# Kernel optimization log

Hardware: AMD Instinct MI355X
Metric: run time of the kernel (lower is better)

The kernel has to match this reference:

```python
import jax, jax.numpy as jnp
import numpy as np

B, W, N = 128, 128, 64
HID = 150  # lstm_hid_dim == recon_hid_dim
L = 2      # layer_numb


def _edges_fc(n):
    # for j in range(n) for i in range(n) if i != j -> row0 = i (src), row1 = j (dst)
    a = np.arange(n)
    src = np.concatenate([np.delete(a, j) for j in range(n)])
    dst = np.repeat(a, n - 1)
    return np.stack([src, dst]).astype(np.int32)


def _edges_tc(w):
    # for j in range(w) for i in range(j) -> row0 = i (src), row1 = j (dst)
    src = np.concatenate([np.arange(j) for j in range(1, w)])
    dst = np.repeat(np.arange(w), np.arange(w))
    return np.stack([src, dst]).astype(np.int32)


def _batch_edges(e, b, n):
    # tile per-graph edges b times with node offsets (block-diagonal batched graph)
    off = (jnp.arange(b) * n).astype(e.dtype)
    return (e[:, None, :] + off[None, :, None]).reshape(2, -1)


def _gat_conv(x, edge_index, w, a_src, a_dst, b):
    # PyG GATConv, heads=1: h = x W^T; e_ij = LeakyReLU(a_src.h_j + a_dst.h_i); softmax over dst
    m = x.shape[0]
    loop = jnp.arange(m, dtype=edge_index.dtype)
    src = jnp.concatenate([edge_index[0], loop])
    dst = jnp.concatenate([edge_index[1], loop])
    h = x @ w.T
    e = jax.nn.leaky_relu(h @ a_src, 0.2)[src] + jax.nn.leaky_relu(jnp.zeros((), h.dtype), 0.2) * 0
    e = jax.nn.leaky_relu((h @ a_src)[src] + (h @ a_dst)[dst], 0.2)
    emax = jax.ops.segment_max(e, dst, num_segments=m)
    ex = jnp.exp(e - emax[dst])
    denom = jax.ops.segment_sum(ex, dst, num_segments=m)
    alpha = ex / denom[dst]
    out = jax.ops.segment_sum(h[src] * alpha[:, None], dst, num_segments=m)
    return out + b


def _gcn_conv(x, edge_index, w, b):
    # PyG GCNConv: add self loops, D^{-1/2} A D^{-1/2} (x W^T) + b
    m = x.shape[0]
    loop = jnp.arange(m, dtype=edge_index.dtype)
    src = jnp.concatenate([edge_index[0], loop])
    dst = jnp.concatenate([edge_index[1], loop])
    h = x @ w.T
    deg = jax.ops.segment_sum(jnp.ones(src.shape, h.dtype), dst, num_segments=m)
    dinv = 1.0 / jnp.sqrt(deg)
    norm = dinv[src] * dinv[dst]
    out = jax.ops.segment_sum(h[src] * norm[:, None], dst, num_segments=m)
    return out + b


def _stgat_block(x, fc_e, tc_e, gw, gas, gad, gb, cw, cb):
    x = jax.lax.stop_gradient(x)  # data.clone().detach()
    b, w, n = x.shape
    xp = jnp.transpose(x, (0, 2, 1)).reshape(-1, w)          # [B*N, W]
    f = jax.nn.relu(_gat_conv(xp, fc_e, gw, gas, gad, gb))
    f = f.reshape(b, n, w)
    z = jnp.transpose(f, (0, 2, 1)).reshape(-1, n)           # [B*W, N]
    t = jax.nn.relu(_gcn_conv(z, tc_e, cw, cb))
    t = t.reshape(b, n, w)  # faithful to torch view(B, node_num, -1) quirk
    return jnp.transpose(t, (0, 2, 1))


def _conv_branch(x, w, b, k):
    pad = (k - 1) // 2
    xc = jnp.transpose(x, (0, 2, 1))  # [B, N, W]
    xc = jnp.pad(xc, ((0, 0), (0, 0), (pad, pad)))
    y = jax.lax.conv_general_dilated(xc, w, (1,), 'VALID',
                                     dimension_numbers=('NCH', 'OIH', 'NCH'))
    y = jax.nn.relu(y + b[None, :, None])
    return jnp.transpose(y, (0, 2, 1))


def _lstm_scan(x, w_ih, w_hh, b_ih, b_hh, reverse):
    hdim = w_hh.shape[1]

    def step(carry, xt):
        h, c = carry
        g = xt @ w_ih.T + h @ w_hh.T + b_ih + b_hh
        i, f, gg, o = jnp.split(g, 4, axis=-1)
        c = jax.nn.sigmoid(f) * c + jax.nn.sigmoid(i) * jnp.tanh(gg)
        h = jax.nn.sigmoid(o) * jnp.tanh(c)
        return (h, c), h

    bsz = x.shape[0]
    init = (jnp.zeros((bsz, hdim), x.dtype), jnp.zeros((bsz, hdim), x.dtype))
    xs = jnp.swapaxes(x, 0, 1)  # [T, B, D]
    _, hs = jax.lax.scan(step, init, xs, reverse=reverse)
    return jnp.swapaxes(hs, 0, 1)  # [B, T, H]


def reference(x, fc_edge_index, tc_edge_index,
              conv2_w, conv2_b, conv3_w, conv3_b,
              gat_w, gat_asrc, gat_adst, gat_b, gcn_w, gcn_b,
              lstm_wih, lstm_whh, lstm_bih, lstm_bhh,
              dec_wih, dec_whh, dec_bih, dec_bhh, fc_w, fc_b):
    b, w, n = x.shape
    fc_e = _batch_edges(fc_edge_index, b, n)
    tc_e = _batch_edges(tc_edge_index, b, w)
    hs = [x, _conv_branch(x, conv2_w, conv2_b, 5), _conv_branch(x, conv3_w, conv3_b, 7)]
    nlayers = gat_w.shape[1]
    for t in range(3):
        for l in range(nlayers):
            hs[t] = hs[t] + _stgat_block(hs[t], fc_e, tc_e,
                                         gat_w[t, l], gat_asrc[t, l], gat_adst[t, l],
                                         gat_b[t, l], gcn_w[t, l], gcn_b[t, l])
    h = jnp.concatenate(hs, axis=2)  # [B, W, 3N]
    fwd = _lstm_scan(h, lstm_wih[0], lstm_whh[0], lstm_bih[0], lstm_bhh[0], False)
    bwd = _lstm_scan(h, lstm_wih[1], lstm_whh[1], lstm_bih[1], lstm_bhh[1], True)
    h_end = jnp.concatenate([fwd[:, -1], bwd[:, -1]], axis=-1)  # [B, 2H]
    rep = jnp.repeat(h_end, w, axis=1).reshape(b, w, -1)  # repeat_interleave + view quirk
    dfwd = _lstm_scan(rep, dec_wih[0], dec_whh[0], dec_bih[0], dec_bhh[0], False)
    dbwd = _lstm_scan(rep, dec_wih[1], dec_whh[1], dec_bih[1], dec_bhh[1], True)
    dec = jnp.concatenate([dfwd, dbwd], axis=-1)  # [B, W, 2H]
    return dec @ fc_w.T + fc_b


def setup_inputs() -> dict:
    key = jax.random.key(0)
    ks = jax.random.split(key, 24)
    s = 0.05
    f = lambda k, shp: jax.random.normal(k, shp, jnp.float32) * s
    return {
        'x': jax.random.normal(ks[0], (B, W, N), jnp.float32),
        'fc_edge_index': jnp.asarray(_edges_fc(N)),
        'tc_edge_index': jnp.asarray(_edges_tc(W)),
        'conv2_w': f(ks[1], (N, N, 5)), 'conv2_b': f(ks[2], (N,)),
        'conv3_w': f(ks[3], (N, N, 7)), 'conv3_b': f(ks[4], (N,)),
        'gat_w': f(ks[5], (3, L, W, W)), 'gat_asrc': f(ks[6], (3, L, W)),
        'gat_adst': f(ks[7], (3, L, W)), 'gat_b': f(ks[8], (3, L, W)),
        'gcn_w': f(ks[9], (3, L, N, N)), 'gcn_b': f(ks[10], (3, L, N)),
        'lstm_wih': f(ks[11], (2, 4 * HID, 3 * N)), 'lstm_whh': f(ks[12], (2, 4 * HID, HID)),
        'lstm_bih': f(ks[13], (2, 4 * HID)), 'lstm_bhh': f(ks[14], (2, 4 * HID)),
        'dec_wih': f(ks[15], (2, 4 * HID, 2 * HID)), 'dec_whh': f(ks[16], (2, 4 * HID, HID)),
        'dec_bih': f(ks[17], (2, 4 * HID)), 'dec_bhh': f(ks[18], (2, 4 * HID)),
        'fc_w': f(ks[19], (N, 2 * HID)), 'fc_b': f(ks[20], (N,)),
    }
```

## Files before the change

kernel.cpp:

```cpp
#include <hip/hip_runtime.h>
#include <hip/hip_fp16.h>


typedef _Float16 v2h __attribute__((ext_vector_type(2)));

__device__ __forceinline__ float sigm(float x) {
    return 1.0f / (1.0f + __expf(-x));
}
__device__ __forceinline__ float tanhfast(float x) {
    return 2.0f / (1.0f + __expf(-2.0f * x)) - 1.0f;
}
__device__ __forceinline__ v2h pk2(float a, float b) {
    v2h r; r[0] = (_Float16)a; r[1] = (_Float16)b; return r;
}
__device__ __forceinline__ unsigned pku(float a, float b) {
    return __builtin_bit_cast(unsigned, pk2(a, b));
}
__device__ __forceinline__ v2h upk(unsigned u) { return __builtin_bit_cast(v2h, u); }
__device__ __forceinline__ float fdot2(v2h a, v2h b, float c) {
#if __has_builtin(__builtin_amdgcn_fdot2)
    return __builtin_amdgcn_fdot2(a, b, c, false);
#else
    return c + (float)a[0] * (float)b[0] + (float)a[1] * (float)b[1];
#endif
}

__device__ __forceinline__ void barrier_lds() {
    asm volatile("s_waitcnt lgkmcnt(0)" ::: "memory");
    __builtin_amdgcn_s_barrier();
}

__global__ void k_copy(const float* __restrict__ x, float* __restrict__ hs0) {
    int i = blockIdx.x * 256 + threadIdx.x;
    ((float4*)hs0)[i] = ((const float4*)x)[i];
}

__global__ __launch_bounds__(256) void k_conv2(
    const float* __restrict__ x,
    const float* __restrict__ cw5, const float* __restrict__ cb5,
    const float* __restrict__ cw7, const float* __restrict__ cb7,
    float* __restrict__ hs1, float* __restrict__ hs2) {
    extern __shared__ float S[];
    float* xt = S;
    float* wl = S + 70 * 68;
    int b = blockIdx.x, wh = blockIdx.y, br = blockIdx.z;
    int K = br ? 7 : 5;
    const float* cw = br ? cw7 : cw5;
    const float* cb = br ? cb7 : cb5;
    float* dst = br ? hs2 : hs1;
    int w0 = wh * 64;
    int tid = threadIdx.x;

    for (int f = tid; f < 70 * 64; f += 256) {
        int ww = f >> 6, i = f & 63;
        int wp = w0 - 3 + ww;
        xt[ww * 68 + i] = ((unsigned)wp < 128u) ? x[b * 8192 + wp * 64 + i] : 0.f;
    }
    int nw = K * 4096;
    for (int f = tid; f < nw; f += 256) {
        int j = f & 3, o = (f >> 2) & 63, i4 = (f >> 8) & 15, t = f >> 12;
        wl[f] = cw[(o * 64 + i4 * 4 + j) * K + t];
    }
    __syncthreads();

    int to = tid & 15, tw = tid >> 4;
    float acc[4][4] = {};
    int ob = 3 - (K >> 1);
    for (int t = 0; t < K; ++t) {
        int rbase = tw * 4 + t + ob;
        for (int i4 = 0; i4 < 16; ++i4) {
            float4 a0 = *(const float4*)&xt[(rbase + 0) * 68 + i4 * 4];
            float4 a1 = *(const float4*)&xt[(rbase + 1) * 68 + i4 * 4];
            float4 a2 = *(const float4*)&xt[(rbase + 2) * 68 + i4 * 4];
            float4 a3 = *(const float4*)&xt[(rbase + 3) * 68 + i4 * 4];
            const float* wrow = &wl[(t * 16 + i4) * 256];
            float4 b0 = *(const float4*)&wrow[to * 4];
            float4 b1 = *(const float4*)&wrow[(to + 16) * 4];
            float4 b2 = *(const float4*)&wrow[(to + 32) * 4];
            float4 b3 = *(const float4*)&wrow[(to + 48) * 4];
            #define DOT4(w_, a_) \
                acc[w_][0] = fmaf(a_.x, b0.x, acc[w_][0]); acc[w_][0] = fmaf(a_.y, b0.y, acc[w_][0]); \
                acc[w_][0] = fmaf(a_.z, b0.z, acc[w_][0]); acc[w_][0] = fmaf(a_.w, b0.w, acc[w_][0]); \
                acc[w_][1] = fmaf(a_.x, b1.x, acc[w_][1]); acc[w_][1] = fmaf(a_.y, b1.y, acc[w_][1]); \
                acc[w_][1] = fmaf(a_.z, b1.z, acc[w_][1]); acc[w_][1] = fmaf(a_.w, b1.w, acc[w_][1]); \
                acc[w_][2] = fmaf(a_.x, b2.x, acc[w_][2]); acc[w_][2] = fmaf(a_.y, b2.y, acc[w_][2]); \
                acc[w_][2] = fmaf(a_.z, b2.z, acc[w_][2]); acc[w_][2] = fmaf(a_.w, b2.w, acc[w_][2]); \
                acc[w_][3] = fmaf(a_.x, b3.x, acc[w_][3]); acc[w_][3] = fmaf(a_.y, b3.y, acc[w_][3]); \
                acc[w_][3] = fmaf(a_.z, b3.z, acc[w_][3]); acc[w_][3] = fmaf(a_.w, b3.w, acc[w_][3]);
            DOT4(0, a0)
            DOT4(1, a1)
            DOT4(2, a2)
            DOT4(3, a3)
            #undef DOT4
        }
    }
    #pragma unroll
    for (int wj = 0; wj < 4; ++wj) {
        int w = w0 + tw * 4 + wj;
        #pragma unroll
        for (int oj = 0; oj < 4; ++oj) {
            int o = to + 16 * oj;
            dst[b * 8192 + w * 64 + o] = fmaxf(acc[wj][oj] + cb[o], 0.f);
        }
    }
}

__global__ __launch_bounds__(256, 2) void k_stgat(
    float* __restrict__ hs0, float* __restrict__ hs1, float* __restrict__ hs2,
    const float* __restrict__ gat_w, const float* __restrict__ gat_asrc,
    const float* __restrict__ gat_adst, const float* __restrict__ gat_b,
    const float* __restrict__ gcn_w, const float* __restrict__ gcn_b, int l) {
    extern __shared__ float S[];
    _Float16* Sh = (_Float16*)S;
    const int XHh = 0;
    const int GHh = 8448;
    const int HHTh = 25344;
    const int AHh = 34560;
    const int FHh = 8448;
    const int CHh = 0;
    const int SDo = 17024;
    const int CSo = 17024;
    const int HGo = 8576;

    int b = blockIdx.x, br = blockIdx.y, tid = threadIdx.x;
    float* hs = (br == 0 ? hs0 : (br == 1 ? hs1 : hs2)) + b * 8192;
    int wsel = br * 2 + l;
    const float* gw = gat_w + wsel * 16384;
    const float* asr = gat_asrc + wsel * 128;
    const float* ads = gat_adst + wsel * 128;
    const float* gb = gat_b + wsel * 128;
    const float* cwp = gcn_w + wsel * 4096;
    const float* cbp = gcn_b + wsel * 64;

    {
        const float4* hsv = (const float4*)hs;
        for (int mt = tid; mt < 512; mt += 256) {
            int ng = mt & 15, wg = mt >> 4;
            float4 r0 = hsv[(wg * 4 + 0) * 16 + ng];
            float4 r1 = hsv[(wg * 4 + 1) * 16 + ng];
            float4 r2 = hsv[(wg * 4 + 2) * 16 + ng];
            float4 r3 = hsv[(wg * 4 + 3) * 16 + ng];
            int n0 = ng * 4, ww = wg * 4;
            *(uint2*)&Sh[XHh + (n0 + 0) * 132 + ww] = make_uint2(pku(r0.x, r1.x), pku(r2.x, r3.x));
            *(uint2*)&Sh[XHh + (n0 + 1) * 132 + ww] = make_uint2(pku(r0.y, r1.y), pku(r2.y, r3.y));
            *(uint2*)&Sh[XHh + (n0 + 2) * 132 + ww] = make_uint2(pku(r0.z, r1.z), pku(r2.z, r3.z));
            *(uint2*)&Sh[XHh + (n0 + 3) * 132 + ww] = make_uint2(pku(r0.w, r1.w), pku(r2.w, r3.w));
        }
        const float4* gwv = (const float4*)gw;
        for (int f4 = tid; f4 < 4096; f4 += 256) {
            float4 v = gwv[f4];
            int wo = f4 >> 5, k4 = f4 & 31;
            *(uint2*)&Sh[GHh + wo * 132 + k4 * 4] = make_uint2(pku(v.x, v.y), pku(v.z, v.w));
        }
    }
    __syncthreads();

    int wq = tid & 15, nq = tid >> 4;
    {
        float asv[8], adv[8];
        #pragma unroll
        for (int c = 0; c < 8; ++c) { asv[c] = asr[wq + 16 * c]; adv[c] = ads[wq + 16 * c]; }
        float acc0[8] = {}, acc1[8] = {}, acc2[8] = {}, acc3[8] = {};
        const _Float16* Arow = Sh + XHh + nq * 4 * 132;
        const _Float16* Brow = Sh + GHh + wq * 132;
        for (int k4 = 0; k4 < 32; ++k4) {
            uint2 u0 = *(const uint2*)&Arow[k4 * 4];
            uint2 u1 = *(const uint2*)&Arow[132 + k4 * 4];
            uint2 u2 = *(const uint2*)&Arow[264 + k4 * 4];
            uint2 u3 = *(const uint2*)&Arow[396 + k4 * 4];
            v2h a0l = upk(u0.x), a0h = upk(u0.y), a1l = upk(u1.x), a1h = upk(u1.y);
            v2h a2l = upk(u2.x), a2h = upk(u2.y), a3l = upk(u3.x), a3h = upk(u3.y);
            #pragma unroll
            for (int c = 0; c < 8; ++c) {
                uint2 ub = *(const uint2*)&Brow[c * (16 * 132) + k4 * 4];
                v2h bl = upk(ub.x), bh = upk(ub.y);
                acc0[c] = fdot2(a0l, bl, acc0[c]); acc0[c] = fdot2(a0h, bh, acc0[c]);
                acc1[c] = fdot2(a1l, bl, acc1[c]); acc1[c] = fdot2(a1h, bh, acc1[c]);
                acc2[c] = fdot2(a2l, bl, acc2[c]); acc2[c] = fdot2(a2h, bh, acc2[c]);
                acc3[c] = fdot2(a3l, bl, acc3[c]); acc3[c] = fdot2(a3h, bh, acc3[c]);
            }
        }
        #pragma unroll
        for (int c = 0; c < 8; ++c)
            *(uint2*)&Sh[HHTh + (wq + 16 * c) * 68 + nq * 4] =
                make_uint2(pku(acc0[c], acc1[c]), pku(acc2[c], acc3[c]));
        float ps0 = 0, ps1 = 0, ps2 = 0, ps3 = 0, pd0 = 0, pd1 = 0, pd2 = 0, pd3 = 0;
        #pragma unroll
        for (int c = 0; c < 8; ++c) {
            ps0 = fmaf(acc0[c], asv[c], ps0); ps1 = fmaf(acc1[c], asv[c], ps1);
            ps2 = fmaf(acc2[c], asv[c], ps2); ps3 = fmaf(acc3[c], asv[c], ps3);
            pd0 = fmaf(acc0[c], adv[c], pd0); pd1 = fmaf(acc1[c], adv[c], pd1);
            pd2 = fmaf(acc2[c], adv[c], pd2); pd3 = fmaf(acc3[c], adv[c], pd3);
        }
        #pragma unroll
        for (int m = 1; m < 16; m <<= 1) {
            ps0 += __shfl_xor(ps0, m); ps1 += __shfl_xor(ps1, m);
            ps2 += __shfl_xor(ps2, m); ps3 += __shfl_xor(ps3, m);
            pd0 += __shfl_xor(pd0, m); pd1 += __shfl_xor(pd1, m);
            pd2 += __shfl_xor(pd2, m); pd3 += __shfl_xor(pd3, m);
        }
        if (wq == 0) {
            S[SDo + nq * 4 + 0] = ps0; S[SDo + nq * 4 + 1] = ps1;
            S[SDo + nq * 4 + 2] = ps2; S[SDo + nq * 4 + 3] = ps3;
            S[SDo + 64 + nq * 4 + 0] = pd0; S[SDo + 64 + nq * 4 + 1] = pd1;
            S[SDo + 64 + nq * 4 + 2] = pd2; S[SDo + 64 + nq * 4 + 3] = pd3;
        }
    }
    __syncthreads();

    {
        const float4* cwv = (const float4*)cwp;
        for (int f4 = tid; f4 < 1024; f4 += 256) {
            float4 v = cwv[f4];
            int c = f4 >> 4, k4 = f4 & 15;
            *(uint2*)&Sh[CHh + c * 68 + k4 * 4] = make_uint2(pku(v.x, v.y), pku(v.z, v.w));
        }
        if (tid < 64) {
            int j = tid;
            float dj = S[SDo + 64 + j];
            float mx = -1e30f;
            for (int i = 0; i < 64; ++i) {
                float e = S[SDo + i] + dj;
                e = (e > 0.f) ? e : 0.2f * e;
                mx = fmaxf(mx, e);
            }
            float sum = 0.f;
            for (int i = 0; i < 64; i += 2) {
                float e0 = S[SDo + i] + dj;     e0 = (e0 > 0.f) ? e0 : 0.2f * e0;
                float e1 = S[SDo + i + 1] + dj; e1 = (e1 > 0.f) ? e1 : 0.2f * e1;
                float x0 = __expf(e0 - mx), x1 = __expf(e1 - mx);
                sum += x0 + x1;
                *(unsigned*)&Sh[AHh + j * 68 + i] = pku(x0, x1);
            }
            float rinv = 1.f / sum;
            for (int i = 0; i < 64; i += 2) {
                v2h v = upk(*(const unsigned*)&Sh[AHh + j * 68 + i]);
                *(unsigned*)&Sh[AHh + j * 68 + i] = pku((float)v[0] * rinv, (float)v[1] * rinv);
            }
        }
    }
    __syncthreads();

    {
        float gbv[8];
        #pragma unroll
        for (int c = 0; c < 8; ++c) gbv[c] = gb[wq + 16 * c];
        float acc0[8] = {}, acc1[8] = {}, acc2[8] = {}, acc3[8] = {};
        const _Float16* Arow = Sh + AHh + nq * 4 * 68;
        const _Float16* Brow = Sh + HHTh + wq * 68;
        for (int k4 = 0; k4 < 16; ++k4) {
            uint2 u0 = *(const uint2*)&Arow[k4 * 4];
            uint2 u1 = *(const uint2*)&Arow[68 + k4 * 4];
            uint2 u2 = *(const uint2*)&Arow[136 + k4 * 4];
            uint2 u3 = *(const uint2*)&Arow[204 + k4 * 4];
            v2h a0l = upk(u0.x), a0h = upk(u0.y), a1l = upk(u1.x), a1h = upk(u1.y);
            v2h a2l = upk(u2.x), a2h = upk(u2.y), a3l = upk(u3.x), a3h = upk(u3.y);
            #pragma unroll
            for (int c = 0; c < 8; ++c) {
                uint2 ub = *(const uint2*)&Brow[c * (16 * 68) + k4 * 4];
                v2h bl = upk(ub.x), bh = upk(ub.y);
                acc0[c] = fdot2(a0l, bl, acc0[c]); acc0[c] = fdot2(a0h, bh, acc0[c]);
                acc1[c] = fdot2(a1l, bl, acc1[c]); acc1[c] = fdot2(a1h, bh, acc1[c]);
                acc2[c] = fdot2(a2l, bl, acc2[c]); acc2[c] = fdot2(a2h, bh, acc2[c]);
                acc3[c] = fdot2(a3l, bl, acc3[c]); acc3[c] = fdot2(a3h, bh, acc3[c]);
            }
        }
        #pragma unroll
        for (int c = 0; c < 8; ++c) {
            float f0 = fmaxf(acc0[c] + gbv[c], 0.f);
            float f1 = fmaxf(acc1[c] + gbv[c], 0.f);
            float f2 = fmaxf(acc2[c] + gbv[c], 0.f);
            float f3 = fmaxf(acc3[c] + gbv[c], 0.f);
            *(uint2*)&Sh[FHh + (wq + 16 * c) * 68 + nq * 4] = make_uint2(pku(f0, f1), pku(f2, f3));
        }
    }
    __syncthreads();

    {
        int cq = tid & 7, wg = tid >> 3;
        float acc0[8] = {}, acc1[8] = {}, acc2[8] = {}, acc3[8] = {};
        const _Float16* Arow = Sh + FHh + wg * 4 * 68;
        const _Float16* Brow = Sh + CHh + cq * 68;
        for (int k4 = 0; k4 < 16; ++k4) {
            uint2 u0 = *(const uint2*)&Arow[k4 * 4];
            uint2 u1 = *(const uint2*)&Arow[68 + k4 * 4];
            uint2 u2 = *(const uint2*)&Arow[136 + k4 * 4];
            uint2 u3 = *(const uint2*)&Arow[204 + k4 * 4];
            v2h a0l = upk(u0.x), a0h = upk(u0.y), a1l = upk(u1.x), a1h = upk(u1.y);
            v2h a2l = upk(u2.x), a2h = upk(u2.y), a3l = upk(u3.x), a3h = upk(u3.y);
            #pragma unroll
            for (int cc = 0; cc < 8; ++cc) {
                uint2 ub = *(const uint2*)&Brow[cc * (8 * 68) + k4 * 4];
                v2h bl = upk(ub.x), bh = upk(ub.y);
                acc0[cc] = fdot2(a0l, bl, acc0[cc]); acc0[cc] = fdot2(a0h, bh, acc0[cc]);
                acc1[cc] = fdot2(a1l, bl, acc1[cc]); acc1[cc] = fdot2(a1h, bh, acc1[cc]);
                acc2[cc] = fdot2(a2l, bl, acc2[cc]); acc2[cc] = fdot2(a2h, bh, acc2[cc]);
                acc3[cc] = fdot2(a3l, bl, acc3[cc]); acc3[cc] = fdot2(a3h, bh, acc3[cc]);
            }
        }
        #pragma unroll
        for (int cc = 0; cc < 8; ++cc) {
            int c = cq + 8 * cc;
            S[HGo + (wg * 4 + 0) * 66 + c] = acc0[cc];
            S[HGo + (wg * 4 + 1) * 66 + c] = acc1[cc];
            S[HGo + (wg * 4 + 2) * 66 + c] = acc2[cc];
            S[HGo + (wg * 4 + 3) * 66 + c] = acc3[cc];
        }
    }
    __syncthreads();

    {
        int c = tid & 63, q = tid >> 6;
        float local = 0.f;
        for (int i = 0; i < 32; ++i) {
            int w = q * 32 + i;
            local = fmaf(rsqrtf((float)(w + 1)), S[HGo + w * 66 + c], local);
        }
        S[CSo + q * 64 + c] = local;
    }
    __syncthreads();
    {
        int c = tid & 63, q = tid >> 6;
        float run = 0.f;
        for (int qq = 0; qq < q; ++qq) run += S[CSo + qq * 64 + c];
        float cbv = cbp[c];
        for (int i = 0; i < 32; ++i) {
            int w = q * 32 + i;
            float dv = rsqrtf((float)(w + 1));
            run = fmaf(dv, S[HGo + w * 66 + c], run);
            S[HGo + w * 66 + c] = fmaxf(fmaf(dv, run, cbv), 0.f);
        }
    }
    __syncthreads();

    {
        float4* hsv4 = (float4*)hs;
        for (int f4 = tid; f4 < 2048; f4 += 256) {
            int a = f4 >> 4, cc0 = (f4 & 15) * 4;
            float4 old = hsv4[f4];
            int n = a & 63, ahi = a >> 6;
            old.x += S[HGo + (cc0 * 2 + ahi) * 66 + n];
            old.y += S[HGo + ((cc0 + 1) * 2 + ahi) * 66 + n];
            old.z += S[HGo + ((cc0 + 2) * 2 + ahi) * 66 + n];
            old.w += S[HGo + ((cc0 + 3) * 2 + ahi) * 66 + n];
            hsv4[f4] = old;
        }
    }
}

__global__ __launch_bounds__(256) void k_encgemm2(
    const float* __restrict__ hs0, const float* __restrict__ hs1, const float* __restrict__ hs2,
    const float* __restrict__ wih, const float* __restrict__ bih, const float* __restrict__ bhh,
    float* __restrict__ gx0) {
    __shared__ __align__(16) _Float16 Xh[128 * 72];
    __shared__ __align__(16) _Float16 Wh[128 * 72];
    int b = blockIdx.x, gy = blockIdx.y, tid = threadIdx.x;
    int g0 = gy * 128;
    int ty = tid >> 4, tx = tid & 15;
    float acc[8][8];
    #pragma unroll
    for (int i = 0; i < 8; ++i)
        #pragma unroll
        for (int j = 0; j < 8; ++j) acc[i][j] = 0.f;
    const float* hsb[3] = {hs0 + b * 8192, hs1 + b * 8192, hs2 + b * 8192};

    for (int c = 0; c < 3; ++c) {
        const float4* src = (const float4*)hsb[c];
        for (int f = tid; f < 2048; f += 256) {
            int t = f >> 4, k4 = f & 15;
            float4 v = src[f];
            int pos = (((k4 >> 1) ^ ((t >> 3) & 7)) << 1) + (k4 & 1);
            *(uint2*)&Xh[t * 72 + pos * 4] = make_uint2(pku(v.x, v.y), pku(v.z, v.w));
        }
        for (int f = tid; f < 2048; f += 256) {
            int g = f >> 4, k4 = f & 15;
            int gg = g0 + g;
            float4 v = (gg < 600) ? *(const float4*)&wih[gg * 192 + c * 64 + k4 * 4]
                                  : make_float4(0.f, 0.f, 0.f, 0.f);
            int pos = (((k4 >> 1) ^ ((g >> 3) & 7)) << 1) + (k4 & 1);
            *(uint2*)&Wh[g * 72 + pos * 4] = make_uint2(pku(v.x, v.y), pku(v.z, v.w));
        }
        __syncthreads();
        #pragma unroll
        for (int k8 = 0; k8 < 8; ++k8) {
            uint4 av[8];
            #pragma unroll
            for (int i = 0; i < 8; ++i) {
                int row = ty * 8 + i;
                av[i] = *(const uint4*)&Xh[row * 72 + (k8 ^ ((row >> 3) & 7)) * 8];
            }
            #pragma unroll
            for (int j = 0; j < 8; ++j) {
                int row = tx * 8 + j;
                uint4 bv = *(const uint4*)&Wh[row * 72 + (k8 ^ ((row >> 3) & 7)) * 8];
                v2h b0 = upk(bv.x), b1 = upk(bv.y), b2 = upk(bv.z), b3 = upk(bv.w);
                #pragma unroll
                for (int i = 0; i < 8; ++i) {
                    acc[i][j] = fdot2(upk(av[i].x), b0, acc[i][j]);
                    acc[i][j] = fdot2(upk(av[i].y), b1, acc[i][j]);
                    acc[i][j] = fdot2(upk(av[i].z), b2, acc[i][j]);
                    acc[i][j] = fdot2(upk(av[i].w), b3, acc[i][j]);
                }
            }
        }
        __syncthreads();
    }
    #pragma unroll
    for (int i = 0; i < 8; ++i) {
        int t = ty * 8 + i;
        float* orow = gx0 + (b * 128 + t) * 600;
        #pragma unroll
        for (int jj = 0; jj < 2; ++jj) {
            int gbase = g0 + tx * 8 + jj * 4;
            if (gbase + 3 < 600) {
                float4 o;
                o.x = acc[i][jj * 4 + 0] + bih[gbase + 0] + bhh[gbase + 0];
                o.y = acc[i][jj * 4 + 1] + bih[gbase + 1] + bhh[gbase + 1];
                o.z = acc[i][jj * 4 + 2] + bih[gbase + 2] + bhh[gbase + 2];
                o.w = acc[i][jj * 4 + 3] + bih[gbase + 3] + bhh[gbase + 3];
                *(float4*)&orow[gbase] = o;
            } else {
                for (int e = 0; e < 4; ++e) {
                    int g = gbase + e;
                    if (g < 600) orow[g] = acc[i][jj * 4 + e] + bih[g] + bhh[g];
                }
            }
        }
    }
}

__global__ void k_encgx1(const float* __restrict__ hs0, const float* __restrict__ hs1,
                         const float* __restrict__ hs2, const float* __restrict__ wih,
                         const float* __restrict__ bih, const float* __restrict__ bhh,
                         float* __restrict__ gx1) {
    __shared__ __align__(16) float sh[192];
    int b = blockIdx.x, tid = threadIdx.x;
    if (tid < 192) {
        const float* src = (tid < 64 ? hs0 : (tid < 128 ? hs1 : hs2));
        sh[tid] = src[b * 8192 + 127 * 64 + (tid & 63)];
    }
    __syncthreads();
    const float* w1 = wih + 600 * 192;
    for (int g = tid; g < 600; g += 256) {
        float acc = bih[600 + g] + bhh[600 + g];
        const float4* wr = (const float4*)(w1 + g * 192);
        #pragma unroll 8
        for (int q = 0; q < 48; ++q) {
            float4 wv = wr[q];
            float4 hv = *(const float4*)&sh[q * 4];
            acc = fmaf(wv.x, hv.x, acc);
            acc = fmaf(wv.y, hv.y, acc);
            acc = fmaf(wv.z, hv.z, acc);
            acc = fmaf(wv.w, hv.w, acc);
        }
        gx1[b * 600 + g] = acc;
    }
}

__global__ void k_ptpref(const float* __restrict__ dwih, float* __restrict__ PT) {
    int dg = blockIdx.x * 256 + threadIdx.x;
    if (dg >= 1200) return;
    const float* wr = dwih + dg * 300;
    float run = 0.f;
    PT[dg] = 0.f;
    for (int k = 0; k < 300; ++k) {
        run += wr[k];
        PT[(k + 1) * 1200 + dg] = run;
    }
}

__global__ void k_pd(const float* __restrict__ PT, float* __restrict__ PD) {
    int id = blockIdx.x * 256 + threadIdx.x;
    if (id >= 153600) return;
    int g = id % 600;
    int tt = id / 600;
    int t = tt & 127, dir = tt >> 7;
    int dg = dir * 600 + g;
    int base = t * 300;
    int j0 = base >> 7;
    int ke1 = (j0 + 1) * 128 - base;
    int ke2 = ke1 + 128; ke2 = ke2 > 300 ? 300 : ke2;
    int ke3 = ke1 + 256; ke3 = ke3 > 300 ? 300 : ke3;
    float p1 = PT[ke1 * 1200 + dg];
    float p2 = PT[ke2 * 1200 + dg];
    float p3 = PT[ke3 * 1200 + dg];
    float p4 = PT[300 * 1200 + dg];
    float4 o = {p1, p2 - p1, p3 - p2, p4 - p3};
    *(float4*)&PD[id * 4] = o;
}

__global__ __launch_bounds__(640, 3) void k_enclstm(
    const float* __restrict__ gx0, const float* __restrict__ gx1,
    const float* __restrict__ whh, float* __restrict__ h_end) {
    int bid = blockIdx.x, t = threadIdx.x;
    if (bid >= 128) {
        int b = bid - 128;
        if (t < 150) {
            float ai = gx1[b * 600 + t];
            float ag = gx1[b * 600 + 300 + t];
            float ao = gx1[b * 600 + 450 + t];
            float c = sigm(ai) * tanhfast(ag);
            h_end[b * 300 + 150 + t] = sigm(ao) * tanhfast(c);
        }
        return;
    }
    __shared__ __align__(16) _Float16 hbuf[2][152];
    int b = bid;
    bool on = t < 600;
    int j = t >> 2, g4 = t & 3;
    int grow = g4 * 150 + j;
    v2h wv[76];
    #pragma unroll
    for (int p = 0; p < 76; ++p) wv[p] = pk2(0.f, 0.f);
    if (on) {
        const float* r = whh + grow * 150;
        #pragma unroll
        for (int p = 0; p < 75; ++p) wv[p] = pk2(r[2 * p], r[2 * p + 1]);
    }
    for (int i = t; i < 304; i += 640) ((_Float16*)hbuf)[i] = (_Float16)0.f;
    float c = 0.f;
    float xc = on ? gx0[(b * 128) * 600 + grow] : 0.f;
    barrier_lds();
    for (int s = 0; s < 128; ++s) {
        float xn = (on && s < 127) ? gx0[(b * 128 + s + 1) * 600 + grow] : 0.f;
        float s0 = 0.f, s1 = 0.f, s2 = 0.f, s3 = 0.f;
        const float4* hp = (const float4*)hbuf[s & 1];
        #pragma unroll
        for (int cc = 0; cc < 19; ++cc) {
            float4 hv = hp[cc];
            s0 = fdot2(wv[4 * cc + 0], __builtin_bit_cast(v2h, hv.x), s0);
            s1 = fdot2(wv[4 * cc + 1], __builtin_bit_cast(v2h, hv.y), s1);
            s2 = fdot2(wv[4 * cc + 2], __builtin_bit_cast(v2h, hv.z), s2);
            s3 = fdot2(wv[4 * cc + 3], __builtin_bit_cast(v2h, hv.w), s3);
        }
        float a = xc + ((s0 + s1) + (s2 + s3));
        bool isg = (g4 == 2);
        float sg = sigm(isg ? 2.f * a : a);
        float act = isg ? fmaf(2.f, sg, -1.f) : sg;
        float vf = __shfl_xor(act, 1);
        float vg = __shfl_xor(act, 2);
        float vo = __shfl_xor(vf, 2);
        if (on && g4 == 0) {
            c = fmaf(vf, c, act * vg);
            float h = vo * tanhfast(c);
            hbuf[(s + 1) & 1][j] = (_Float16)h;
            if (s == 127) h_end[b * 300 + j] = h;
        }
        xc = xn;
        barrier_lds();
    }
}

__global__ __launch_bounds__(640, 3) void k_declstm(
    const float* __restrict__ PD, const float* __restrict__ hend,
    const float* __restrict__ whh_all, const float* __restrict__ bih,
    const float* __restrict__ bhh, _Float16* __restrict__ dec_out) {
    __shared__ __align__(16) float she[304];
    __shared__ __align__(16) _Float16 hbuf[2][152];
    int dir = blockIdx.x >> 7, b = blockIdx.x & 127;
    int t = threadIdx.x;
    bool on = t < 600;
    int j = t >> 2, g4 = t & 3;
    int grow = g4 * 150 + j;
    v2h wv[76];
    #pragma unroll
    for (int p = 0; p < 76; ++p) wv[p] = pk2(0.f, 0.f);
    float bias = 0.f;
    if (on) {
        const float* r = whh_all + dir * 90000 + grow * 150;
        #pragma unroll
        for (int p = 0; p < 75; ++p) wv[p] = pk2(r[2 * p], r[2 * p + 1]);
        bias = bih[dir * 600 + grow] + bhh[dir * 600 + grow];
    }
    for (int i = t; i < 304; i += 640) she[i] = (i < 300) ? hend[b * 300 + i] : 0.f;
    for (int i = t; i < 304; i += 640) ((_Float16*)hbuf)[i] = (_Float16)0.f;
    float c = 0.f;
    int t0 = dir ? 127 : 0;
    float4 pd = {0.f, 0.f, 0.f, 0.f};
    if (on) pd = *(const float4*)&PD[((dir * 128 + t0) * 600 + grow) * 4];
    barrier_lds();
    for (int s = 0; s < 128; ++s) {
        int tt = dir ? (127 - s) : s;
        float4 pdn = {0.f, 0.f, 0.f, 0.f};
        if (on && s < 127) {
            int tn = dir ? (126 - s) : (s + 1);
            pdn = *(const float4*)&PD[((dir * 128 + tn) * 600 + grow) * 4];
        }
        int j0 = (tt * 300) >> 7;
        float e0 = she[j0], e1 = she[j0 + 1], e2 = she[j0 + 2], e3 = she[j0 + 3];
        float a = bias + e0 * pd.x + e1 * pd.y + e2 * pd.z + e3 * pd.w;
        float s0 = 0.f, s1 = 0.f, s2 = 0.f, s3 = 0.f;
        const float4* hp = (const float4*)hbuf[s & 1];
        #pragma unroll
        for (int cc = 0; cc < 19; ++cc) {
            float4 hv = hp[cc];
            s0 = fdot2(wv[4 * cc + 0], __builtin_bit_cast(v2h, hv.x), s0);
            s1 = fdot2(wv[4 * cc + 1], __builtin_bit_cast(v2h, hv.y), s1);
            s2 = fdot2(wv[4 * cc + 2], __builtin_bit_cast(v2h, hv.z), s2);
            s3 = fdot2(wv[4 * cc + 3], __builtin_bit_cast(v2h, hv.w), s3);
        }
        a += (s0 + s1) + (s2 + s3);
        bool isg = (g4 == 2);
        float sg = sigm(isg ? 2.f * a : a);
        float act = isg ? fmaf(2.f, sg, -1.f) : sg;
        float vf = __shfl_xor(act, 1);
        float vg = __shfl_xor(act, 2);
        float vo = __shfl_xor(vf, 2);
        if (on && g4 == 0) {
            c = fmaf(vf, c, act * vg);
            float h = vo * tanhfast(c);
            hbuf[(s + 1) & 1][j] = (_Float16)h;
            dec_out[(b * 128 + tt) * 300 + dir * 150 + j] = (_Float16)h;
        }
        pd = pdn;
        barrier_lds();
    }
}

__global__ __launch_bounds__(256) void k_fingemm(const _Float16* __restrict__ decH,
                                                 const float* __restrict__ fw,
                                                 const float* __restrict__ fb,
                                                 float* __restrict__ out) {
    __shared__ __align__(16) unsigned AsT[16 * 68];
    __shared__ __align__(16) unsigned FwT[16 * 68];
    int r0 = blockIdx.x * 64, tid = threadIdx.x;
    int ty = tid >> 4, tx = tid & 15;
    float acc[4][4];
    #pragma unroll
    for (int r = 0; r < 4; ++r)
        #pragma unroll
        for (int c = 0; c < 4; ++c) acc[r][c] = 0.f;
    for (int kc = 0; kc < 10; ++kc) {
        int k0 = kc * 32;
        for (int f = tid; f < 1024; f += 256) {
            int m = f >> 4, kk2 = f & 15;
            int k = k0 + kk2 * 2;
            AsT[kk2 * 68 + m] =
                (k + 1 < 300) ? *(const unsigned*)&decH[(r0 + m) * 300 + k] : 0u;
        }
        for (int f = tid; f < 1024; f += 256) {
            int n = f >> 4, kk2 = f & 15;
            int k = k0 + kk2 * 2;
            FwT[kk2 * 68 + n] =
                (k + 1 < 300) ? pku(fw[n * 300 + k], fw[n * 300 + k + 1]) : 0u;
        }
        __syncthreads();
        #pragma unroll 4
        for (int kk2 = 0; kk2 < 16; ++kk2) {
            uint4 a4 = *(const uint4*)&AsT[kk2 * 68 + ty * 4];
            uint4 w4 = *(const uint4*)&FwT[kk2 * 68 + tx * 4];
            v2h a0 = upk(a4.x), a1 = upk(a4.y), a2 = upk(a4.z), a3 = upk(a4.w);
            v2h w0 = upk(w4.x), w1 = upk(w4.y), w2 = upk(w4.z), w3 = upk(w4.w);
            acc[0][0] = fdot2(a0, w0, acc[0][0]); acc[0][1] = fdot2(a0, w1, acc[0][1]);
            acc[0][2] = fdot2(a0, w2, acc[0][2]); acc[0][3] = fdot2(a0, w3, acc[0][3]);
            acc[1][0] = fdot2(a1, w0, acc[1][0]); acc[1][1] = fdot2(a1, w1, acc[1][1]);
            acc[1][2] = fdot2(a1, w2, acc[1][2]); acc[1][3] = fdot2(a1, w3, acc[1][3]);
            acc[2][0] = fdot2(a2, w0, acc[2][0]); acc[2][1] = fdot2(a2, w1, acc[2][1]);
            acc[2][2] = fdot2(a2, w2, acc[2][2]); acc[2][3] = fdot2(a2, w3, acc[2][3]);
            acc[3][0] = fdot2(a3, w0, acc[3][0]); acc[3][1] = fdot2(a3, w1, acc[3][1]);
            acc[3][2] = fdot2(a3, w2, acc[3][2]); acc[3][3] = fdot2(a3, w3, acc[3][3]);
        }
        __syncthreads();
    }
    for (int r = 0; r < 4; ++r) {
        int m = r0 + ty * 4 + r;
        float4 o4;
        o4.x = acc[r][0] + fb[tx * 4 + 0];
        o4.y = acc[r][1] + fb[tx * 4 + 1];
        o4.z = acc[r][2] + fb[tx * 4 + 2];
        o4.w = acc[r][3] + fb[tx * 4 + 3];
        *(float4*)&out[m * 64 + tx * 4] = o4;
    }
}

extern "C" void kernel_launch(void* const* d_in, const int* in_sizes, int n_in,
                              void* d_out, int out_size, void* d_ws, size_t ws_size,
                              hipStream_t stream) {
    const float* x = (const float*)d_in[0];
    const float* c2w = (const float*)d_in[3];
    const float* c2b = (const float*)d_in[4];
    const float* c3w = (const float*)d_in[5];
    const float* c3b = (const float*)d_in[6];
    const float* gatw = (const float*)d_in[7];
    const float* gatas = (const float*)d_in[8];
    const float* gatad = (const float*)d_in[9];
    const float* gatb = (const float*)d_in[10];
    const float* gcnw = (const float*)d_in[11];
    const float* gcnb = (const float*)d_in[12];
    const float* lwih = (const float*)d_in[13];
    const float* lwhh = (const float*)d_in[14];
    const float* lbih = (const float*)d_in[15];
    const float* lbhh = (const float*)d_in[16];
    const float* dwih = (const float*)d_in[17];
    const float* dwhh = (const float*)d_in[18];
    const float* dbih = (const float*)d_in[19];
    const float* dbhh = (const float*)d_in[20];
    const float* fcw = (const float*)d_in[21];
    const float* fcb = (const float*)d_in[22];
    float* out = (float*)d_out;
    float* ws = (float*)d_ws;

    float* hs0 = ws;
    float* hs1 = ws + 1048576;
    float* hs2 = ws + 2097152;
    float* gx0 = ws + 3145728;
    float* gx1 = ws + 12976128;
    float* hend = ws + 13052928;
    float* PT = ws + 13091328;
    _Float16* decH = (_Float16*)(ws + 13452528);
    float* PD = hs0;

    k_copy<<<1024, 256, 0, stream>>>(x, hs0);
    k_conv2<<<dim3(128, 2, 2), 256, (70 * 68 + 7 * 16 * 256) * 4, stream>>>(
        x, c2w, c2b, c3w, c3b, hs1, hs2);
    for (int l = 0; l < 2; ++l)
        k_stgat<<<dim3(128, 3), 256, 77824, stream>>>(hs0, hs1, hs2, gatw, gatas,
                                                      gatad, gatb, gcnw, gcnb, l);
    k_encgemm2<<<dim3(128, 5), 256, 0, stream>>>(hs0, hs1, hs2, lwih, lbih, lbhh, gx0);
    k_encgx1<<<128, 256, 0, stream>>>(hs0, hs1, hs2, lwih, lbih, lbhh, gx1);
    k_ptpref<<<5, 256, 0, stream>>>(dwih, PT);
    k_pd<<<600, 256, 0, stream>>>(PT, PD);
    k_enclstm<<<256, 640, 0, stream>>>(gx0, gx1, lwhh, hend);
    k_declstm<<<256, 640, 0, stream>>>(PD, hend, dwhh, dbih, dbhh, decH);
    k_fingemm<<<256, 256, 0, stream>>>(decH, fcw, fcb, out);
}
```

Baseline: 543.0 us.

## Batch LSTM recurrences over 16 sequences per block using MFMA f16

Replaces the per-sequence fdot2 LSTM recurrences (one block per batch element) with blocks that process 16 batch rows at once and compute the hidden-to-gate product with mfma_f32_16x16x32_f16, using recurrent weights pre-packed into MFMA fragment layout by a new prep kernel. The encoder input-gate buffer is rewritten into a padded, gate-interleaved layout, and the decoder input gates are precomputed into an f16 buffer by a new kernel. The aim is to move the sequential recurrence work onto matrix cores. In exchange, the recurrent kernels launch only 8 or 16 blocks, which leaves most CUs idle, and the change adds extra kernels, extra memory traffic and f16 storage of the decoder gate inputs.

```diff
diff --git a/kernel.cpp b/kernel.cpp
--- a/kernel.cpp
+++ b/kernel.cpp
@@ -3,6 +3,8 @@
 
 
 typedef _Float16 v2h __attribute__((ext_vector_type(2)));
+typedef _Float16 v8h __attribute__((ext_vector_type(8)));
+typedef float v4f __attribute__((ext_vector_type(4)));
 
 __device__ __forceinline__ float sigm(float x) {
     return 1.0f / (1.0f + __expf(-x));
@@ -351,7 +353,7 @@
 __global__ __launch_bounds__(256) void k_encgemm2(
     const float* __restrict__ hs0, const float* __restrict__ hs1, const float* __restrict__ hs2,
     const float* __restrict__ wih, const float* __restrict__ bih, const float* __restrict__ bhh,
-    float* __restrict__ gx0) {
+    float* __restrict__ gx0p) {
     __shared__ __align__(16) _Float16 Xh[128 * 72];
     __shared__ __align__(16) _Float16 Wh[128 * 72];
     int b = blockIdx.x, gy = blockIdx.y, tid = threadIdx.x;
@@ -408,25 +410,26 @@
     #pragma unroll
     for (int i = 0; i < 8; ++i) {
         int t = ty * 8 + i;
-        float* orow = gx0 + (b * 128 + t) * 600;
-        #pragma unroll
-        for (int jj = 0; jj < 2; ++jj) {
-            int gbase = g0 + tx * 8 + jj * 4;
-            if (gbase + 3 < 600) {
-                float4 o;
-                o.x = acc[i][jj * 4 + 0] + bih[gbase + 0] + bhh[gbase + 0];
-                o.y = acc[i][jj * 4 + 1] + bih[gbase + 1] + bhh[gbase + 1];
-                o.z = acc[i][jj * 4 + 2] + bih[gbase + 2] + bhh[gbase + 2];
-                o.w = acc[i][jj * 4 + 3] + bih[gbase + 3] + bhh[gbase + 3];
-                *(float4*)&orow[gbase] = o;
-            } else {
-                for (int e = 0; e < 4; ++e) {
-                    int g = gbase + e;
-                    if (g < 600) orow[g] = acc[i][jj * 4 + e] + bih[g] + bhh[g];
-                }
-            }
-        }
-    }
+        float* orow = gx0p + (b * 128 + t) * 640;
+        #pragma unroll
+        for (int j = 0; j < 8; ++j) {
+            int g = g0 + tx * 8 + j;
+            if (g < 600) {
+                int q = (g >= 450) ? 3 : (g >= 300) ? 2 : (g >= 150) ? 1 : 0;
+                int u = g - q * 150;
+                int col = ((u >> 4) << 6) + (q << 4) + (u & 15);
+                orow[col] = acc[i][j] + bih[g] + bhh[g];
+            }
+        }
+    }
+}
+
+__global__ void k_zpad(float* __restrict__ gx0p) {
+    int f = blockIdx.x * 256 + threadIdx.x;
+    if (f >= 655360) return;
+    int pidx = f % 40, bt = f / 40;
+    int ct = pidx / 10, ul = 6 + pidx % 10;
+    gx0p[bt * 640 + 576 + ct * 16 + ul] = 0.f;
 }
 
 __global__ void k_encgx1(const float* __restrict__ hs0, const float* __restrict__ hs1,
@@ -489,12 +492,61 @@
     *(float4*)&PD[id * 4] = o;
 }
 
-__global__ __launch_bounds__(640, 3) void k_enclstm(
-    const float* __restrict__ gx0, const float* __restrict__ gx1,
-    const float* __restrict__ whh, float* __restrict__ h_end) {
-    int bid = blockIdx.x, t = threadIdx.x;
-    if (bid >= 128) {
-        int b = bid - 128;
+__global__ void k_prepB(const float* __restrict__ whh, _Float16* __restrict__ Bp, int ndir) {
+    int f = blockIdx.x * 256 + threadIdx.x;
+    int per = 102400;
+    if (f >= per * ndir) return;
+    int dir = f / per, r = f % per;
+    int j = r & 7, rest = r >> 3;
+    int lane = rest & 63; rest >>= 6;
+    int ct = rest & 3; rest >>= 2;
+    int kt = rest % 5, w = rest / 5;
+    int u = 16 * w + (lane & 15);
+    int k = kt * 32 + 8 * (lane >> 4) + j;
+    float v = (u < 150 && k < 150) ? whh[dir * 90000 + (ct * 150 + u) * 150 + k] : 0.f;
+    Bp[f] = (_Float16)v;
+}
+
+__global__ __launch_bounds__(256) void k_gxd(
+    const float* __restrict__ PD, const float* __restrict__ hend,
+    const float* __restrict__ dbih, const float* __restrict__ dbhh,
+    _Float16* __restrict__ gxd) {
+    __shared__ float PDs[2400 + 600];
+    int dt = blockIdx.x, tid = threadIdx.x;
+    int dir = dt >> 7, t = dt & 127;
+    for (int g = tid; g < 600; g += 256) {
+        float4 p = *(const float4*)&PD[((dir * 128 + t) * 600 + g) * 4];
+        *(float4*)&PDs[g * 4] = p;
+        PDs[2400 + g] = dbih[dir * 600 + g] + dbhh[dir * 600 + g];
+    }
+    __syncthreads();
+    int j0 = (t * 300) >> 7;
+    for (int b = 0; b < 128; ++b) {
+        float e0 = hend[b * 300 + j0];
+        float e1 = (j0 + 1 < 300) ? hend[b * 300 + j0 + 1] : 0.f;
+        float e2 = (j0 + 2 < 300) ? hend[b * 300 + j0 + 2] : 0.f;
+        float e3 = (j0 + 3 < 300) ? hend[b * 300 + j0 + 3] : 0.f;
+        _Float16* orow = gxd + (((dir * 128 + b) * 128) + t) * 640;
+        for (int col = tid; col < 640; col += 256) {
+            int u = 16 * (col >> 6) + (col & 15);
+            int q = (col >> 4) & 3;
+            float v = 0.f;
+            if (u < 150) {
+                int g = q * 150 + u;
+                const float* p = &PDs[g * 4];
+                v = PDs[2400 + g] + e0 * p[0] + e1 * p[1] + e2 * p[2] + e3 * p[3];
+            }
+            orow[col] = (_Float16)v;
+        }
+    }
+}
+
+__global__ __launch_bounds__(640) void k_enclstm_m(
+    const float* __restrict__ gx0p, const float* __restrict__ gx1,
+    const _Float16* __restrict__ BpE, float* __restrict__ h_end) {
+    int bid = blockIdx.x, tid = threadIdx.x;
+    if (bid >= 8) {
+        int b = bid - 8, t = tid;
         if (t < 150) {
             float ai = gx1[b * 600 + t];
             float ag = gx1[b * 600 + 300 + t];
@@ -504,115 +556,107 @@
         }
         return;
     }
-    __shared__ __align__(16) _Float16 hbuf[2][152];
-    int b = bid;
-    bool on = t < 600;
-    int j = t >> 2, g4 = t & 3;
-    int grow = g4 * 150 + j;
-    v2h wv[76];
+    __shared__ __align__(16) _Float16 hA[2][5][512];
+    int b0 = bid * 16;
+    int w = tid >> 6, l = tid & 63;
+    v8h Bf[5][4];
     #pragma unroll
-    for (int p = 0; p < 76; ++p) wv[p] = pk2(0.f, 0.f);
-    if (on) {
-        const float* r = whh + grow * 150;
-        #pragma unroll
-        for (int p = 0; p < 75; ++p) wv[p] = pk2(r[2 * p], r[2 * p + 1]);
-    }
-    for (int i = t; i < 304; i += 640) ((_Float16*)hbuf)[i] = (_Float16)0.f;
-    float c = 0.f;
-    float xc = on ? gx0[(b * 128) * 600 + grow] : 0.f;
+    for (int kt = 0; kt < 5; ++kt)
+        #pragma unroll
+        for (int ct = 0; ct < 4; ++ct)
+            Bf[kt][ct] = *(const v8h*)(BpE + (((w * 5 + kt) * 4 + ct) * 64 + l) * 8);
+    for (int i = tid; i < 5120; i += 640) ((_Float16*)hA)[i] = (_Float16)0.f;
+    float cst[4] = {0.f, 0.f, 0.f, 0.f};
+    int row0 = 4 * (l >> 4);
+    int u = 16 * w + (l & 15);
+    int kloc = u & 31, tile = u >> 5;
+    int wl2 = ((row0 & 15)) | ((kloc >> 3) << 4);
+    const float* gpb = gx0p + ((long)(b0 + row0) * 128) * 640 + w * 64 + (l & 15);
     barrier_lds();
     for (int s = 0; s < 128; ++s) {
-        float xn = (on && s < 127) ? gx0[(b * 128 + s + 1) * 600 + grow] : 0.f;
-        float s0 = 0.f, s1 = 0.f, s2 = 0.f, s3 = 0.f;
-        const float4* hp = (const float4*)hbuf[s & 1];
-        #pragma unroll
-        for (int cc = 0; cc < 19; ++cc) {
-            float4 hv = hp[cc];
-            s0 = fdot2(wv[4 * cc + 0], __builtin_bit_cast(v2h, hv.x), s0);
-            s1 = fdot2(wv[4 * cc + 1], __builtin_bit_cast(v2h, hv.y), s1);
-            s2 = fdot2(wv[4 * cc + 2], __builtin_bit_cast(v2h, hv.z), s2);
-            s3 = fdot2(wv[4 * cc + 3], __builtin_bit_cast(v2h, hv.w), s3);
-        }
-        float a = xc + ((s0 + s1) + (s2 + s3));
-        bool isg = (g4 == 2);
-        float sg = sigm(isg ? 2.f * a : a);
-        float act = isg ? fmaf(2.f, sg, -1.f) : sg;
-        float vf = __shfl_xor(act, 1);
-        float vg = __shfl_xor(act, 2);
-        float vo = __shfl_xor(vf, 2);
-        if (on && g4 == 0) {
-            c = fmaf(vf, c, act * vg);
-            float h = vo * tanhfast(c);
-            hbuf[(s + 1) & 1][j] = (_Float16)h;
-            if (s == 127) h_end[b * 300 + j] = h;
-        }
-        xc = xn;
+        v4f acc[4];
+        #pragma unroll
+        for (int ct = 0; ct < 4; ++ct) {
+            #pragma unroll
+            for (int reg = 0; reg < 4; ++reg)
+                acc[ct][reg] = gpb[(long)reg * 81920 + (long)s * 640 + ct * 16];
+        }
+        #pragma unroll
+        for (int kt = 0; kt < 5; ++kt) {
+            v8h Af = *(const v8h*)&hA[s & 1][kt][l * 8];
+            acc[0] = __builtin_amdgcn_mfma_f32_16x16x32_f16(Af, Bf[kt][0], acc[0], 0, 0, 0);
+            acc[1] = __builtin_amdgcn_mfma_f32_16x16x32_f16(Af, Bf[kt][1], acc[1], 0, 0, 0);
+            acc[2] = __builtin_amdgcn_mfma_f32_16x16x32_f16(Af, Bf[kt][2], acc[2], 0, 0, 0);
+            acc[3] = __builtin_amdgcn_mfma_f32_16x16x32_f16(Af, Bf[kt][3], acc[3], 0, 0, 0);
+        }
+        _Float16* hw = &hA[(s + 1) & 1][tile][0];
+        #pragma unroll
+        for (int reg = 0; reg < 4; ++reg) {
+            float iv = sigm(acc[0][reg]);
+            float fv = sigm(acc[1][reg]);
+            float gv = tanhfast(acc[2][reg]);
+            float ov = sigm(acc[3][reg]);
+            cst[reg] = fmaf(fv, cst[reg], iv * gv);
+            float h = ov * tanhfast(cst[reg]);
+            hw[(wl2 + reg) * 8 + (kloc & 7)] = (_Float16)h;
+            if (s == 127 && u < 150) h_end[(b0 + row0 + reg) * 300 + u] = h;
+        }
         barrier_lds();
     }
 }
 
-__global__ __launch_bounds__(640, 3) void k_declstm(
-    const float* __restrict__ PD, const float* __restrict__ hend,
-    const float* __restrict__ whh_all, const float* __restrict__ bih,
-    const float* __restrict__ bhh, _Float16* __restrict__ dec_out) {
-    __shared__ __align__(16) float she[304];
-    __shared__ __align__(16) _Float16 hbuf[2][152];
-    int dir = blockIdx.x >> 7, b = blockIdx.x & 127;
-    int t = threadIdx.x;
-    bool on = t < 600;
-    int j = t >> 2, g4 = t & 3;
-    int grow = g4 * 150 + j;
-    v2h wv[76];
+__global__ __launch_bounds__(640) void k_declstm_m(
+    const _Float16* __restrict__ gxd, const _Float16* __restrict__ BpD,
+    _Float16* __restrict__ decH) {
+    __shared__ __align__(16) _Float16 hA[2][5][512];
+    int bid = blockIdx.x, tid = threadIdx.x;
+    int dir = bid >> 3, b0 = (bid & 7) * 16;
+    int w = tid >> 6, l = tid & 63;
+    v8h Bf[5][4];
     #pragma unroll
-    for (int p = 0; p < 76; ++p) wv[p] = pk2(0.f, 0.f);
-    float bias = 0.f;
-    if (on) {
-        const float* r = whh_all + dir * 90000 + grow * 150;
-        #pragma unroll
-        for (int p = 0; p < 75; ++p) wv[p] = pk2(r[2 * p], r[2 * p + 1]);
-        bias = bih[dir * 600 + grow] + bhh[dir * 600 + grow];
-    }
-    for (int i = t; i < 304; i += 640) she[i] = (i < 300) ? hend[b * 300 + i] : 0.f;
-    for (int i = t; i < 304; i += 640) ((_Float16*)hbuf)[i] = (_Float16)0.f;
-    float c = 0.f;
-    int t0 = dir ? 127 : 0;
-    float4 pd = {0.f, 0.f, 0.f, 0.f};
-    if (on) pd = *(const float4*)&PD[((dir * 128 + t0) * 600 + grow) * 4];
+    for (int kt = 0; kt < 5; ++kt)
+        #pragma unroll
+        for (int ct = 0; ct < 4; ++ct)
+            Bf[kt][ct] = *(const v8h*)(BpD + (long)dir * 102400 +
+                                       (((w * 5 + kt) * 4 + ct) * 64 + l) * 8);
+    for (int i = tid; i < 5120; i += 640) ((_Float16*)hA)[i] = (_Float16)0.f;
+    float cst[4] = {0.f, 0.f, 0.f, 0.f};
+    int row0 = 4 * (l >> 4);
+    int u = 16 * w + (l & 15);
+    int kloc = u & 31, tile = u >> 5;
+    int wl2 = (row0 & 15) | ((kloc >> 3) << 4);
+    const _Float16* gpb = gxd + ((long)((dir * 128 + b0 + row0)) * 128) * 640 + w * 64 + (l & 15);
     barrier_lds();
     for (int s = 0; s < 128; ++s) {
-        int tt = dir ? (127 - s) : s;
-        float4 pdn = {0.f, 0.f, 0.f, 0.f};
-        if (on && s < 127) {
-            int tn = dir ? (126 - s) : (s + 1);
-            pdn = *(const float4*)&PD[((dir * 128 + tn) * 600 + grow) * 4];
-        }
-        int j0 = (tt * 300) >> 7;
-        float e0 = she[j0], e1 = she[j0 + 1], e2 = she[j0 + 2], e3 = she[j0 + 3];
-        float a = bias + e0 * pd.x + e1 * pd.y + e2 * pd.z + e3 * pd.w;
-        float s0 = 0.f, s1 = 0.f, s2 = 0.f, s3 = 0.f;
-        const float4* hp = (const float4*)hbuf[s & 1];
-        #pragma unroll
-        for (int cc = 0; cc < 19; ++cc) {
-            float4 hv = hp[cc];
-            s0 = fdot2(wv[4 * cc + 0], __builtin_bit_cast(v2h, hv.x), s0);
-            s1 = fdot2(wv[4 * cc + 1], __builtin_bit_cast(v2h, hv.y), s1);
-            s2 = fdot2(wv[4 * cc + 2], __builtin_bit_cast(v2h, hv.z), s2);
-            s3 = fdot2(wv[4 * cc + 3], __builtin_bit_cast(v2h, hv.w), s3);
-        }
-        a += (s0 + s1) + (s2 + s3);
-        bool isg = (g4 == 2);
-        float sg = sigm(isg ? 2.f * a : a);
-        float act = isg ? fmaf(2.f, sg, -1.f) : sg;
-        float vf = __shfl_xor(act, 1);
-        float vg = __shfl_xor(act, 2);
-        float vo = __shfl_xor(vf, 2);
-        if (on && g4 == 0) {
-            c = fmaf(vf, c, act * vg);
-            float h = vo * tanhfast(c);
-            hbuf[(s + 1) & 1][j] = (_Float16)h;
-            dec_out[(b * 128 + tt) * 300 + dir * 150 + j] = (_Float16)h;
-        }
-        pd = pdn;
+        int t = dir ? (127 - s) : s;
+        v4f acc[4];
+        #pragma unroll
+        for (int ct = 0; ct < 4; ++ct) {
+            #pragma unroll
+            for (int reg = 0; reg < 4; ++reg)
+                acc[ct][reg] = (float)gpb[(long)reg * 81920 + (long)t * 640 + ct * 16];
+        }
+        #pragma unroll
+        for (int kt = 0; kt < 5; ++kt) {
+            v8h Af = *(const v8h*)&hA[s & 1][kt][l * 8];
+            acc[0] = __builtin_amdgcn_mfma_f32_16x16x32_f16(Af, Bf[kt][0], acc[0], 0, 0, 0);
+            acc[1] = __builtin_amdgcn_mfma_f32_16x16x32_f16(Af, Bf[kt][1], acc[1], 0, 0, 0);
+            acc[2] = __builtin_amdgcn_mfma_f32_16x16x32_f16(Af, Bf[kt][2], acc[2], 0, 0, 0);
+            acc[3] = __builtin_amdgcn_mfma_f32_16x16x32_f16(Af, Bf[kt][3], acc[3], 0, 0, 0);
+        }
+        _Float16* hw = &hA[(s + 1) & 1][tile][0];
+        #pragma unroll
+        for (int reg = 0; reg < 4; ++reg) {
+            float iv = sigm(acc[0][reg]);
+            float fv = sigm(acc[1][reg]);
+            float gv = tanhfast(acc[2][reg]);
+            float ov = sigm(acc[3][reg]);
+            cst[reg] = fmaf(fv, cst[reg], iv * gv);
+            float h = ov * tanhfast(cst[reg]);
+            hw[(wl2 + reg) * 8 + (kloc & 7)] = (_Float16)h;
+            if (u < 150)
+                decH[((b0 + row0 + reg) * 128 + t) * 300 + dir * 150 + u] = (_Float16)h;
+        }
         barrier_lds();
     }
 }
@@ -703,24 +747,31 @@
     float* hs0 = ws;
     float* hs1 = ws + 1048576;
     float* hs2 = ws + 2097152;
-    float* gx0 = ws + 3145728;
-    float* gx1 = ws + 12976128;
-    float* hend = ws + 13052928;
-    float* PT = ws + 13091328;
-    _Float16* decH = (_Float16*)(ws + 13452528);
+    float* gx0p = ws + 3145728;
+    float* gx1 = ws + 13631488;
+    float* hend = ws + 13708288;
+    float* PT = ws + 13746688;
+    _Float16* decH = (_Float16*)(ws + 14107888);
+    _Float16* BpE = (_Float16*)(ws + 16565488);
+    _Float16* BpD = (_Float16*)(ws + 16616688);
     float* PD = hs0;
-
+    _Float16* gxd = (_Float16*)gx0p;
+
+    k_prepB<<<400, 256, 0, stream>>>(lwhh, BpE, 1);
+    k_prepB<<<800, 256, 0, stream>>>(dwhh, BpD, 2);
     k_copy<<<1024, 256, 0, stream>>>(x, hs0);
     k_conv2<<<dim3(128, 2, 2), 256, (70 * 68 + 7 * 16 * 256) * 4, stream>>>(
         x, c2w, c2b, c3w, c3b, hs1, hs2);
     for (int l = 0; l < 2; ++l)
         k_stgat<<<dim3(128, 3), 256, 77824, stream>>>(hs0, hs1, hs2, gatw, gatas,
                                                       gatad, gatb, gcnw, gcnb, l);
-    k_encgemm2<<<dim3(128, 5), 256, 0, stream>>>(hs0, hs1, hs2, lwih, lbih, lbhh, gx0);
+    k_encgemm2<<<dim3(128, 5), 256, 0, stream>>>(hs0, hs1, hs2, lwih, lbih, lbhh, gx0p);
+    k_zpad<<<2560, 256, 0, stream>>>(gx0p);
     k_encgx1<<<128, 256, 0, stream>>>(hs0, hs1, hs2, lwih, lbih, lbhh, gx1);
     k_ptpref<<<5, 256, 0, stream>>>(dwih, PT);
     k_pd<<<600, 256, 0, stream>>>(PT, PD);
-    k_enclstm<<<256, 640, 0, stream>>>(gx0, gx1, lwhh, hend);
-    k_declstm<<<256, 640, 0, stream>>>(PD, hend, dwhh, dbih, dbhh, decH);
+    k_enclstm_m<<<136, 640, 0, stream>>>(gx0p, gx1, BpE, hend);
+    k_gxd<<<256, 256, 0, stream>>>(PD, hend, dbih, dbhh, gxd);
+    k_declstm_m<<<16, 640, 0, stream>>>(gxd, BpD, decH);
     k_fingemm<<<256, 256, 0, stream>>>(decH, fcw, fcb, out);
 }
```

New measurement: 1.047 ms. +92.9%, slower.
